# Optimization experiments

Hardware: AMD Instinct MI355X
Metric: run time of the kernel (lower is better)

The kernel has to match this reference:

```python
import jax, jax.numpy as jnp
import numpy as np

EMBED = 2048
T = 2048  # max_seq_length
BATCH = 2  # hardcoded by the module's initial-state shape


def setup_inputs() -> dict:
    key = jax.random.key(0)
    ks = jax.random.split(key, 7)
    s = 0.02
    return {
        "x": jax.random.normal(ks[0], (BATCH, EMBED), dtype=jnp.float32),
        "W_ih": jax.random.normal(ks[1], (4 * EMBED, EMBED), dtype=jnp.float32) * s,
        "W_hh": jax.random.normal(ks[2], (4 * EMBED, EMBED), dtype=jnp.float32) * s,
        "b_ih": jax.random.normal(ks[3], (4 * EMBED,), dtype=jnp.float32) * s,
        "b_hh": jax.random.normal(ks[4], (4 * EMBED,), dtype=jnp.float32) * s,
        "W_out": jax.random.normal(ks[5], (EMBED, EMBED), dtype=jnp.float32) * s,
        "b_out": jax.random.normal(ks[6], (EMBED,), dtype=jnp.float32) * s,
    }


def reference(x, W_ih, W_hh, b_ih, b_hh, W_out, b_out):
    E = x.shape[-1]

    def step(carry, _):
        inp, h, c = carry  # each [B, E]
        gates = inp @ W_ih.T + b_ih + h @ W_hh.T + b_hh  # [B, 4E]
        i, f, g, o = jnp.split(gates, 4, axis=-1)  # PyTorch gate order i,f,g,o
        c_new = jax.nn.sigmoid(f) * c + jax.nn.sigmoid(i) * jnp.tanh(g)
        h_new = jax.nn.sigmoid(o) * jnp.tanh(c_new)
        # output of single-layer LSTM == h_new; it is fed back as next input
        return (h_new, h_new, c_new), h_new

    h0 = jnp.zeros((x.shape[0], E), dtype=x.dtype)
    c0 = jnp.zeros((x.shape[0], E), dtype=x.dtype)
    _, seq = jax.lax.scan(step, (x, h0, c0), None, length=T)  # [T, B, E]

    out = seq @ W_out.T + b_out  # dropout is identity in eval
    return jnp.transpose(out, (1, 0, 2))  # [B, T, E]
```

## Files before the change

### kernel.cpp

```cpp
#include <hip/hip_runtime.h>
#include <hip/hip_fp16.h>
#include <stdint.h>


#define E 2048
#define NBLK 256
#define NTHR 512
#define HLDS_B 2304
#define PLS_STRIDE 20
#define PLS_PAR 640
#define SMEM_MAIN 23680
#define SMEM_PROJ 131072

typedef uint32_t u32;
typedef unsigned long long u64;

__device__ __forceinline__ float sigf(float x){
  return __builtin_amdgcn_rcpf(1.0f + __expf(-x));
}
__device__ __forceinline__ float tanhfast(float x){
  float e = __expf(2.0f * x);
  return 1.0f - 2.0f * __builtin_amdgcn_rcpf(e + 1.0f);
}

#define ROWFMA8(W0, W1, W2, W3, A0, A1) \
  A0 = fmaf(__low2float(W0),  p0.x, A0); A0 = fmaf(__high2float(W0), p0.y, A0); \
  A0 = fmaf(__low2float(W1),  p0.z, A0); A0 = fmaf(__high2float(W1), p0.w, A0); \
  A0 = fmaf(__low2float(W2),  p1.x, A0); A0 = fmaf(__high2float(W2), p1.y, A0); \
  A0 = fmaf(__low2float(W3),  p1.z, A0); A0 = fmaf(__high2float(W3), p1.w, A0); \
  A1 = fmaf(__low2float(W0),  q0.x, A1); A1 = fmaf(__high2float(W0), q0.y, A1); \
  A1 = fmaf(__low2float(W1),  q0.z, A1); A1 = fmaf(__high2float(W1), q0.w, A1); \
  A1 = fmaf(__low2float(W2),  q1.x, A1); A1 = fmaf(__high2float(W2), q1.y, A1); \
  A1 = fmaf(__low2float(W3),  q1.z, A1); A1 = fmaf(__high2float(W3), q1.w, A1);

#define POLLCHK(J, UJ) \
  if (pend & (1 << J)){ \
    if ((u32)(UJ >> 32) == tag){ \
      hlds[cdst[J]] = __uint_as_float((u32)UJ); \
      pend &= ~(1 << J); \
    } \
  }

#define ISSUE8(R0, R1, R2, R3, R4, R5, R6, R7) \
  asm volatile( \
    "global_load_dwordx2 %0, %8, off sc0 sc1\n\t" \
    "global_load_dwordx2 %1, %8, off offset:512 sc0 sc1\n\t" \
    "global_load_dwordx2 %2, %8, off offset:1024 sc0 sc1\n\t" \
    "global_load_dwordx2 %3, %8, off offset:1536 sc0 sc1\n\t" \
    "global_load_dwordx2 %4, %8, off offset:2048 sc0 sc1\n\t" \
    "global_load_dwordx2 %5, %8, off offset:2560 sc0 sc1\n\t" \
    "global_load_dwordx2 %6, %8, off offset:3072 sc0 sc1\n\t" \
    "global_load_dwordx2 %7, %8, off offset:3584 sc0 sc1" \
    : "=&v"(R0), "=&v"(R1), "=&v"(R2), "=&v"(R3), \
      "=&v"(R4), "=&v"(R5), "=&v"(R6), "=&v"(R7) \
    : "v"(src) : "memory")

__global__ void __launch_bounds__(NTHR, 1) lstm_kernel(
    const float* __restrict__ xin, const float* __restrict__ Wih,
    const float* __restrict__ Whh, const float* __restrict__ bih,
    const float* __restrict__ bhh, u64* __restrict__ chk,
    float* __restrict__ seqout)
{
  extern __shared__ char smem[];
  float* hlds = (float*)smem;
  float* pls  = (float*)(smem + 18432);
  float* bias = (float*)(smem + 23552);

  const int tid  = threadIdx.x;
  const int blk  = blockIdx.x;
  const int e0   = blk << 3;
  const int lane = tid & 63;
  const int wv   = tid >> 6;
  const int rg   = lane >> 3;
  const int ksl  = lane & 7;
  const int ks   = (wv << 3) + ksl;
  const int k0   = ks << 5;

  if (tid < 32){
    const int grow = ((tid >> 3) << 11) + e0 + (tid & 7);
    bias[tid] = bih[grow] + bhh[grow];
  }
  for (int i = tid; i < 2 * E; i += NTHR){
    const int b = i >> 11, k = i & 2047;
    hlds[b * HLDS_B + (k >> 5) * 36 + (k & 31)] = xin[i];
  }
  __syncthreads();

  const float* hb0 = hlds + ks * 36;
  const float* hb1 = hlds + HLDS_B + ks * 36;

  __half2 wh[64];
  float acc0[4] = {0.f, 0.f, 0.f, 0.f};
  float acc1[4] = {0.f, 0.f, 0.f, 0.f};
  #pragma unroll
  for (int rr = 0; rr < 4; ++rr){
    const int row  = (rg << 2) + rr;
    const int grow = ((row >> 3) << 11) + e0 + (row & 7);
    const float* pa = Wih + (size_t)grow * E + k0;
    const float* pb = Whh + (size_t)grow * E + k0;
    #pragma unroll
    for (int c = 0; c < 8; ++c){
      float4 a = *(const float4*)(pa + (c << 2));
      float4 b = *(const float4*)(pb + (c << 2));
      wh[(rr << 4) + (c << 1)    ] =
        __halves2half2(__float2half_rn(a.x + b.x), __float2half_rn(a.y + b.y));
      wh[(rr << 4) + (c << 1) + 1] =
        __halves2half2(__float2half_rn(a.z + b.z), __float2half_rn(a.w + b.w));
      float4 x0 = *(const float4*)(hb0 + (c << 2));
      float4 x1 = *(const float4*)(hb1 + (c << 2));
      acc0[rr] = fmaf(a.x, x0.x, acc0[rr]); acc0[rr] = fmaf(a.y, x0.y, acc0[rr]);
      acc0[rr] = fmaf(a.z, x0.z, acc0[rr]); acc0[rr] = fmaf(a.w, x0.w, acc0[rr]);
      acc1[rr] = fmaf(a.x, x1.x, acc1[rr]); acc1[rr] = fmaf(a.y, x1.y, acc1[rr]);
      acc1[rr] = fmaf(a.z, x1.z, acc1[rr]); acc1[rr] = fmaf(a.w, x1.w, acc1[rr]);
    }
  }

  const float br = bias[lane & 31];
  float creg = 0.0f;

  int cdst[8];
  #pragma unroll
  for (int j = 0; j < 8; ++j){
    const int c = (wv << 9) + (j << 6) + lane;
    const int b = (c >> 3) & 1;
    const int e = ((c >> 4) << 3) | (c & 7);
    cdst[j] = b * HLDS_B + (e >> 5) * 36 + (e & 31);
  }
  u64* const pchk0 = chk;
  u64* const pchk1 = chk + 4096;

  for (int t = 0; t < 2048; ++t){
    #pragma unroll
    for (int m = 1; m <= 4; m <<= 1){
      #pragma unroll
      for (int rr = 0; rr < 4; ++rr){
        acc0[rr] += __shfl_xor(acc0[rr], m, 64);
        acc1[rr] += __shfl_xor(acc1[rr], m, 64);
      }
    }
    if (ksl == 0){
      float2* pw = (float2*)(pls + (t & 1) * PLS_PAR);
      #pragma unroll
      for (int rr = 0; rr < 4; ++rr)
        pw[((rg << 2) + rr) * (PLS_STRIDE / 2) + wv] = make_float2(acc0[rr], acc1[rr]);
    }
    __syncthreads();

    if (wv == 0){
      const int r = lane & 31;
      const int b = lane >> 5;
      const float* rp = pls + (t & 1) * PLS_PAR + r * PLS_STRIDE;
      float4 v0 = *(const float4*)(rp);
      float4 v1 = *(const float4*)(rp + 4);
      float4 v2 = *(const float4*)(rp + 8);
      float4 v3 = *(const float4*)(rp + 12);
      float s = br + (b ? (v0.y + v0.w + v1.y + v1.w + v2.y + v2.w + v3.y + v3.w)
                        : (v0.x + v0.z + v1.x + v1.z + v2.x + v2.z + v3.x + v3.z));
      const float gi = s;
      const float gf = __shfl(s, (lane + 8)  & 63, 64);
      const float gg = __shfl(s, (lane + 16) & 63, 64);
      const float go = __shfl(s, (lane + 24) & 63, 64);
      if (r < 8){
        const float cn = sigf(gf) * creg + sigf(gi) * tanhfast(gg);
        const float hn = sigf(go) * tanhfast(cn);
        creg = cn;
        if (t < 2047){
          const u64 pk = ((u64)(u32)(t + 1) << 32) | (u64)__float_as_uint(hn);
          u64* dst = (((t + 1) & 1) ? pchk1 : pchk0) + (blk << 4) + (b << 3) + r;
          asm volatile("global_store_dwordx2 %0, %1, off sc0 sc1"
                       :: "v"(dst), "v"(pk) : "memory");
        }
        seqout[(((size_t)b << 11) + (size_t)t) * E + e0 + r] = hn;
      }
    }
    if (t == 2047) break;

    {
      const u64* src = (((t + 1) & 1) ? pchk1 : pchk0) + (wv << 9) + lane;
      const u32 tag = (u32)(t + 1);
      u64 a0_, a1_, a2_, a3_, a4_, a5_, a6_, a7_;
      u64 b0_, b1_, b2_, b3_, b4_, b5_, b6_, b7_;
      ISSUE8(a0_, a1_, a2_, a3_, a4_, a5_, a6_, a7_);
      ISSUE8(b0_, b1_, b2_, b3_, b4_, b5_, b6_, b7_);
      int pend = 0xFF;
      for (;;){
        asm volatile("s_waitcnt vmcnt(8)" ::: "memory");
        POLLCHK(0, a0_) POLLCHK(1, a1_) POLLCHK(2, a2_) POLLCHK(3, a3_)
        POLLCHK(4, a4_) POLLCHK(5, a5_) POLLCHK(6, a6_) POLLCHK(7, a7_)
        if (!pend) break;
        ISSUE8(a0_, a1_, a2_, a3_, a4_, a5_, a6_, a7_);
        asm volatile("s_waitcnt vmcnt(8)" ::: "memory");
        POLLCHK(0, b0_) POLLCHK(1, b1_) POLLCHK(2, b2_) POLLCHK(3, b3_)
        POLLCHK(4, b4_) POLLCHK(5, b5_) POLLCHK(6, b6_) POLLCHK(7, b7_)
        if (!pend) break;
        ISSUE8(b0_, b1_, b2_, b3_, b4_, b5_, b6_, b7_);
      }
      asm volatile("s_waitcnt vmcnt(0)"
        :: "v"(a0_), "v"(a1_), "v"(a2_), "v"(a3_),
           "v"(a4_), "v"(a5_), "v"(a6_), "v"(a7_),
           "v"(b0_), "v"(b1_), "v"(b2_), "v"(b3_),
           "v"(b4_), "v"(b5_), "v"(b6_), "v"(b7_) : "memory");
      asm volatile("s_waitcnt lgkmcnt(0)" ::: "memory");
      __builtin_amdgcn_sched_barrier(0);
    }

    #pragma unroll
    for (int rr = 0; rr < 4; ++rr){ acc0[rr] = 0.f; acc1[rr] = 0.f; }
    #pragma unroll
    for (int c8 = 0; c8 < 4; ++c8){
      float4 p0 = *(const float4*)(hb0 + (c8 << 3));
      float4 p1 = *(const float4*)(hb0 + (c8 << 3) + 4);
      float4 q0 = *(const float4*)(hb1 + (c8 << 3));
      float4 q1 = *(const float4*)(hb1 + (c8 << 3) + 4);
      #pragma unroll
      for (int rr = 0; rr < 4; ++rr){
        ROWFMA8(wh[(rr << 4) + (c8 << 2)],     wh[(rr << 4) + (c8 << 2) + 1],
                wh[(rr << 4) + (c8 << 2) + 2], wh[(rr << 4) + (c8 << 2) + 3],
                acc0[rr], acc1[rr]);
      }
    }
  }
}

__global__ void __launch_bounds__(256, 1) proj_kernel(
    float* __restrict__ io, const float* __restrict__ Wout,
    const float* __restrict__ bout)
{
  extern __shared__ char smem[];
  float* alds = (float*)smem;
  const int tid = threadIdx.x;
  const size_t rbase = (size_t)blockIdx.x * 16 * E;

  for (int idx = tid; idx < 8192; idx += 256){
    float4 v = *(const float4*)(io + rbase + ((size_t)idx << 2));
    *(float4*)(alds + (idx << 2)) = v;
  }
  __syncthreads();

  for (int p = 0; p < 4; ++p){
    const int n0 = (p << 8) + tid;
    const int n1 = n0 + 1024;
    const float* wr0 = Wout + (size_t)n0 * E;
    const float* wr1 = Wout + (size_t)n1 * E;
    float acc0[16], acc1[16];
    #pragma unroll
    for (int m = 0; m < 16; ++m){ acc0[m] = 0.0f; acc1[m] = 0.0f; }
    for (int kc = 0; kc < 256; ++kc){
      const float4 a0v = *(const float4*)(wr0 + (kc << 3));
      const float4 a1v = *(const float4*)(wr0 + (kc << 3) + 4);
      const float4 b0v = *(const float4*)(wr1 + (kc << 3));
      const float4 b1v = *(const float4*)(wr1 + (kc << 3) + 4);
      const float* ap = alds + (kc << 3);
      #pragma unroll
      for (int m = 0; m < 16; ++m){
        const float* a = ap + (m << 11);
        float4 x0 = *(const float4*)(a);
        float4 x1 = *(const float4*)(a + 4);
        acc0[m] = fmaf(a0v.x, x0.x, acc0[m]); acc0[m] = fmaf(a0v.y, x0.y, acc0[m]);
        acc0[m] = fmaf(a0v.z, x0.z, acc0[m]); acc0[m] = fmaf(a0v.w, x0.w, acc0[m]);
        acc0[m] = fmaf(a1v.x, x1.x, acc0[m]); acc0[m] = fmaf(a1v.y, x1.y, acc0[m]);
        acc0[m] = fmaf(a1v.z, x1.z, acc0[m]); acc0[m] = fmaf(a1v.w, x1.w, acc0[m]);
        acc1[m] = fmaf(b0v.x, x0.x, acc1[m]); acc1[m] = fmaf(b0v.y, x0.y, acc1[m]);
        acc1[m] = fmaf(b0v.z, x0.z, acc1[m]); acc1[m] = fmaf(b0v.w, x0.w, acc1[m]);
        acc1[m] = fmaf(b1v.x, x1.x, acc1[m]); acc1[m] = fmaf(b1v.y, x1.y, acc1[m]);
        acc1[m] = fmaf(b1v.z, x1.z, acc1[m]); acc1[m] = fmaf(b1v.w, x1.w, acc1[m]);
      }
    }
    const float bo0 = bout[n0];
    const float bo1 = bout[n1];
    #pragma unroll
    for (int m = 0; m < 16; ++m){
      io[rbase + ((size_t)m << 11) + n0] = acc0[m] + bo0;
      io[rbase + ((size_t)m << 11) + n1] = acc1[m] + bo1;
    }
  }
}

extern "C" void kernel_launch(void* const* d_in, const int* in_sizes, int n_in,
                              void* d_out, int out_size, void* d_ws, size_t ws_size,
                              hipStream_t stream)
{
  const float* xin  = (const float*)d_in[0];
  const float* Wih  = (const float*)d_in[1];
  const float* Whh  = (const float*)d_in[2];
  const float* bih  = (const float*)d_in[3];
  const float* bhh  = (const float*)d_in[4];
  const float* Wout = (const float*)d_in[5];
  const float* bout = (const float*)d_in[6];
  float* out = (float*)d_out;

  u64* chk = (u64*)d_ws;

  hipFuncSetAttribute((const void*)lstm_kernel,
                      hipFuncAttributeMaxDynamicSharedMemorySize, SMEM_MAIN);
  hipFuncSetAttribute((const void*)proj_kernel,
                      hipFuncAttributeMaxDynamicSharedMemorySize, SMEM_PROJ);

  void* args[] = { (void*)&xin, (void*)&Wih, (void*)&Whh, (void*)&bih, (void*)&bhh,
                   (void*)&chk, (void*)&out };
  hipLaunchCooperativeKernel((const void*)lstm_kernel, dim3(NBLK), dim3(NTHR),
                             args, SMEM_MAIN, stream);

  proj_kernel<<<256, 256, SMEM_PROJ, stream>>>(out, Wout, bout);
}
```

Measured before the change: 9.502 ms.

## Poll only pending flags with sleep; widen projection to four outputs per thread

The LSTM inter-block wait loop drops the double-buffered 16-load polling. It now issues one batch of 8 loads, then re-loads only the entries still pending, with an s_sleep between rounds. This cuts memory traffic and contention on the checkpoint flags, at the cost of higher latency per poll round. Separately, the projection kernel computes four output columns per thread instead of two, halving the passes so each LDS activation read is reused by more FMAs, at the cost of more registers.

New measurement: 8.163 ms. -14.1%, faster.

```diff
diff --git a/kernel.cpp b/kernel.cpp
--- a/kernel.cpp
+++ b/kernel.cpp
@@ -54,6 +54,12 @@
     : "=&v"(R0), "=&v"(R1), "=&v"(R2), "=&v"(R3), \
       "=&v"(R4), "=&v"(R5), "=&v"(R6), "=&v"(R7) \
     : "v"(src) : "memory")
+
+#define RELOAD(J, UJ, OFS) \
+  if (pend & (1 << J)){ \
+    asm volatile("global_load_dwordx2 %0, %1, off offset:" OFS " sc0 sc1" \
+                 : "=v"(UJ) : "v"(src) : "memory"); \
+  }
 
 __global__ void __launch_bounds__(NTHR, 1) lstm_kernel(
     const float* __restrict__ xin, const float* __restrict__ Wih,
@@ -179,27 +185,20 @@
       const u64* src = (((t + 1) & 1) ? pchk1 : pchk0) + (wv << 9) + lane;
       const u32 tag = (u32)(t + 1);
       u64 a0_, a1_, a2_, a3_, a4_, a5_, a6_, a7_;
-      u64 b0_, b1_, b2_, b3_, b4_, b5_, b6_, b7_;
       ISSUE8(a0_, a1_, a2_, a3_, a4_, a5_, a6_, a7_);
-      ISSUE8(b0_, b1_, b2_, b3_, b4_, b5_, b6_, b7_);
+      asm volatile("s_waitcnt vmcnt(0)" ::: "memory");
       int pend = 0xFF;
-      for (;;){
-        asm volatile("s_waitcnt vmcnt(8)" ::: "memory");
+      while (true){
         POLLCHK(0, a0_) POLLCHK(1, a1_) POLLCHK(2, a2_) POLLCHK(3, a3_)
         POLLCHK(4, a4_) POLLCHK(5, a5_) POLLCHK(6, a6_) POLLCHK(7, a7_)
-        if (!pend) break;
-        ISSUE8(a0_, a1_, a2_, a3_, a4_, a5_, a6_, a7_);
-        asm volatile("s_waitcnt vmcnt(8)" ::: "memory");
-        POLLCHK(0, b0_) POLLCHK(1, b1_) POLLCHK(2, b2_) POLLCHK(3, b3_)
-        POLLCHK(4, b4_) POLLCHK(5, b5_) POLLCHK(6, b6_) POLLCHK(7, b7_)
-        if (!pend) break;
-        ISSUE8(b0_, b1_, b2_, b3_, b4_, b5_, b6_, b7_);
-      }
-      asm volatile("s_waitcnt vmcnt(0)"
-        :: "v"(a0_), "v"(a1_), "v"(a2_), "v"(a3_),
-           "v"(a4_), "v"(a5_), "v"(a6_), "v"(a7_),
-           "v"(b0_), "v"(b1_), "v"(b2_), "v"(b3_),
-           "v"(b4_), "v"(b5_), "v"(b6_), "v"(b7_) : "memory");
+        if (pend == 0) break;
+        __builtin_amdgcn_s_sleep(1);
+        RELOAD(0, a0_, "0")    RELOAD(1, a1_, "512")
+        RELOAD(2, a2_, "1024") RELOAD(3, a3_, "1536")
+        RELOAD(4, a4_, "2048") RELOAD(5, a5_, "2560")
+        RELOAD(6, a6_, "3072") RELOAD(7, a7_, "3584")
+        asm volatile("s_waitcnt vmcnt(0)" ::: "memory");
+      }
       asm volatile("s_waitcnt lgkmcnt(0)" ::: "memory");
       __builtin_amdgcn_sched_barrier(0);
     }
@@ -237,19 +236,29 @@
   }
   __syncthreads();
 
-  for (int p = 0; p < 4; ++p){
-    const int n0 = (p << 8) + tid;
-    const int n1 = n0 + 1024;
+  for (int p = 0; p < 2; ++p){
+    const int n0 = (p << 10) + tid;
+    const int n1 = n0 + 256;
+    const int n2 = n0 + 512;
+    const int n3 = n0 + 768;
     const float* wr0 = Wout + (size_t)n0 * E;
     const float* wr1 = Wout + (size_t)n1 * E;
-    float acc0[16], acc1[16];
-    #pragma unroll
-    for (int m = 0; m < 16; ++m){ acc0[m] = 0.0f; acc1[m] = 0.0f; }
+    const float* wr2 = Wout + (size_t)n2 * E;
+    const float* wr3 = Wout + (size_t)n3 * E;
+    float acc0[16], acc1[16], acc2[16], acc3[16];
+    #pragma unroll
+    for (int m = 0; m < 16; ++m){
+      acc0[m] = 0.0f; acc1[m] = 0.0f; acc2[m] = 0.0f; acc3[m] = 0.0f;
+    }
     for (int kc = 0; kc < 256; ++kc){
       const float4 a0v = *(const float4*)(wr0 + (kc << 3));
       const float4 a1v = *(const float4*)(wr0 + (kc << 3) + 4);
       const float4 b0v = *(const float4*)(wr1 + (kc << 3));
       const float4 b1v = *(const float4*)(wr1 + (kc << 3) + 4);
+      const float4 c0v = *(const float4*)(wr2 + (kc << 3));
+      const float4 c1v = *(const float4*)(wr2 + (kc << 3) + 4);
+      const float4 d0v = *(const float4*)(wr3 + (kc << 3));
+      const float4 d1v = *(const float4*)(wr3 + (kc << 3) + 4);
       const float* ap = alds + (kc << 3);
       #pragma unroll
       for (int m = 0; m < 16; ++m){
@@ -264,14 +273,26 @@
         acc1[m] = fmaf(b0v.z, x0.z, acc1[m]); acc1[m] = fmaf(b0v.w, x0.w, acc1[m]);
         acc1[m] = fmaf(b1v.x, x1.x, acc1[m]); acc1[m] = fmaf(b1v.y, x1.y, acc1[m]);
         acc1[m] = fmaf(b1v.z, x1.z, acc1[m]); acc1[m] = fmaf(b1v.w, x1.w, acc1[m]);
+        acc2[m] = fmaf(c0v.x, x0.x, acc2[m]); acc2[m] = fmaf(c0v.y, x0.y, acc2[m]);
+        acc2[m] = fmaf(c0v.z, x0.z, acc2[m]); acc2[m] = fmaf(c0v.w, x0.w, acc2[m]);
+        acc2[m] = fmaf(c1v.x, x1.x, acc2[m]); acc2[m] = fmaf(c1v.y, x1.y, acc2[m]);
+        acc2[m] = fmaf(c1v.z, x1.z, acc2[m]); acc2[m] = fmaf(c1v.w, x1.w, acc2[m]);
+        acc3[m] = fmaf(d0v.x, x0.x, acc3[m]); acc3[m] = fmaf(d0v.y, x0.y, acc3[m]);
+        acc3[m] = fmaf(d0v.z, x0.z, acc3[m]); acc3[m] = fmaf(d0v.w, x0.w, acc3[m]);
+        acc3[m] = fmaf(d1v.x, x1.x, acc3[m]); acc3[m] = fmaf(d1v.y, x1.y, acc3[m]);
+        acc3[m] = fmaf(d1v.z, x1.z, acc3[m]); acc3[m] = fmaf(d1v.w, x1.w, acc3[m]);
       }
     }
     const float bo0 = bout[n0];
     const float bo1 = bout[n1];
+    const float bo2 = bout[n2];
+    const float bo3 = bout[n3];
     #pragma unroll
     for (int m = 0; m < 16; ++m){
       io[rbase + ((size_t)m << 11) + n0] = acc0[m] + bo0;
       io[rbase + ((size_t)m << 11) + n1] = acc1[m] + bo1;
+      io[rbase + ((size_t)m << 11) + n2] = acc2[m] + bo2;
+      io[rbase + ((size_t)m << 11) + n3] = acc3[m] + bo3;
     }
   }
 }
```
